# Performance work log

Hardware: AMD Instinct MI355X
Metric: run time of the kernel (lower is better)

The kernel has to match this reference:

```python
import jax, jax.numpy as jnp
import numpy as np

DIM, DEPTH, HEADS = 1024, 6, 16
B, N = 2, 1024
QB = 128.0   # 8-bit activation absmax quant: Qb = 2**(8-1)
EPS = 1e-5


def setup_inputs() -> dict:
    key = jax.random.key(0)
    ks = jax.random.split(key, 4)
    x = jax.random.normal(ks[0], (B, N, DIM), dtype=jnp.float32)
    # BitLinear weights (per layer, two per FFN block), latent fp weights
    ff_w1 = jax.random.normal(ks[1], (DEPTH, DIM, DIM), dtype=jnp.float32) * 0.02
    ff_w2 = jax.random.normal(ks[2], (DEPTH, DIM, DIM), dtype=jnp.float32) * 0.02
    # LayerNorm params (inside FeedForward) and final norm
    ff_ln_g = jnp.ones((DEPTH, DIM), jnp.float32)
    ff_ln_b = jnp.zeros((DEPTH, DIM), jnp.float32)
    final_ln_g = jnp.ones((DIM,), jnp.float32)
    final_ln_b = jnp.zeros((DIM,), jnp.float32)
    return dict(x=x, ff_ln_g=ff_ln_g, ff_ln_b=ff_ln_b, ff_w1=ff_w1,
                ff_w2=ff_w2, final_ln_g=final_ln_g, final_ln_b=final_ln_b)


def layernorm(x, g, b):
    m = jnp.mean(x, axis=-1, keepdims=True)
    v = jnp.mean((x - m) ** 2, axis=-1, keepdims=True)
    return (x - m) * jax.lax.rsqrt(v + EPS) * g + b


def bitlinear(x, w):
    # BitNet b1: binarize weights around their mean, absmax-quantize activations to 8 bits,
    # int-style matmul, then rescale by beta*gamma/Qb.
    alpha = jnp.mean(w)
    w_b = jnp.sign(w - alpha)                 # ternary/binary weights {-1,0,+1}
    beta = jnp.mean(jnp.abs(w))               # ||W||_1 / (n*m)
    gamma = jnp.max(jnp.abs(x))               # activation absmax
    x_q = jnp.clip(x * (QB / gamma), -QB + EPS, QB - EPS)
    y = jnp.einsum('...i,oi->...o', x_q, w_b)
    return y * (beta * gamma / QB)


def attend(x):
    # non-flash multi-head self-attention, q=k=v=x (Attend has no projections)
    b, n, d = x.shape
    dh = d // HEADS
    q = x.reshape(b, n, HEADS, dh).transpose(0, 2, 1, 3)          # bhnd
    scores = jnp.einsum('bhid,bhjd->bhij', q, q) * (dh ** -0.5)   # [B,H,N,N]
    attn = jax.nn.softmax(scores, axis=-1)
    out = jnp.einsum('bhij,bhjd->bhid', attn, q)
    return out.transpose(0, 2, 1, 3).reshape(b, n, d)


def reference(x, ff_ln_g, ff_ln_b, ff_w1, ff_w2, final_ln_g, final_ln_b):
    for i in range(DEPTH):
        x = attend(x) + x
        h = layernorm(x, ff_ln_g[i], ff_ln_b[i])
        h = bitlinear(h, ff_w1[i])
        h = jax.nn.gelu(h, approximate=False)   # torch nn.GELU default = exact
        h = bitlinear(h, ff_w2[i])
        x = h + x
    return layernorm(x, final_ln_g, final_ln_b)
```

## Files before the change

### kernel.cpp

```cpp
#include <hip/hip_runtime.h>
#include <math.h>

typedef __attribute__((ext_vector_type(4))) float f32x4;
typedef __attribute__((ext_vector_type(8))) _Float16 f16x8;

__device__ __forceinline__ f32x4 mfma16h(f16x8 a, f16x8 b, f32x4 c){
  return __builtin_amdgcn_mfma_f32_16x16x32_f16(a, b, c, 0, 0, 0);
}
__device__ __forceinline__ void gload_lds16(const void* g, void* l){
  __builtin_amdgcn_global_load_lds((const __attribute__((address_space(1))) void*)g,
                                   (__attribute__((address_space(3))) void*)l, 16, 0, 0);
}

__global__ __launch_bounds__(256) void k_wstats(const float* __restrict__ w1, const float* __restrict__ w2,
                                                double* __restrict__ dsum, double* __restrict__ dabs){
  const int mat = blockIdx.y;
  const float* wp = (mat < 6) ? (w1 + (size_t)mat*1048576) : (w2 + (size_t)(mat-6)*1048576);
  const f32x4* wv = (const f32x4*)wp + (size_t)blockIdx.x*8192;
  double s = 0.0, a = 0.0;
  for (int j = 0; j < 32; j++){
    f32x4 v = wv[j*256 + threadIdx.x];
    s += (double)v.x + (double)v.y + (double)v.z + (double)v.w;
    a += (double)fabsf(v.x) + (double)fabsf(v.y) + (double)fabsf(v.z) + (double)fabsf(v.w);
  }
  for (int d = 1; d < 64; d <<= 1){ s += __shfl_xor(s, d); a += __shfl_xor(a, d); }
  __shared__ double red[8];
  const int w = threadIdx.x >> 6;
  if ((threadIdx.x & 63) == 0){ red[w*2] = s; red[w*2+1] = a; }
  __syncthreads();
  if (threadIdx.x == 0){
    double S = red[0]+red[2]+red[4]+red[6], A = red[1]+red[3]+red[5]+red[7];
    atomicAdd(&dsum[mat], S);
    atomicAdd(&dabs[mat], A);
  }
}

__global__ __launch_bounds__(256) void k_binarize(const float* __restrict__ w1, const float* __restrict__ w2,
                                                  const double* __restrict__ dsum, _Float16* __restrict__ wb){
  const int blk = blockIdx.x;
  const int mat = blk >> 9;
  const float alpha = (float)(dsum[mat] * (1.0/1048576.0));
  const float* wp = (mat < 6) ? (w1 + (size_t)mat*1048576) : (w2 + (size_t)(mat-6)*1048576);
  const size_t off = (size_t)(blk & 511)*2048 + (size_t)threadIdx.x*8;
  const int n = (int)(off >> 10), k = (int)(off & 1023);
  f32x4 v0 = *(const f32x4*)(wp + off), v1 = *(const f32x4*)(wp + off + 4);
  float vv[8] = {v0.x,v0.y,v0.z,v0.w,v1.x,v1.y,v1.z,v1.w};
  f16x8 pk;
  #pragma unroll
  for (int e = 0; e < 8; e++){
    float d = vv[e] - alpha;
    pk[e] = d > 0.f ? (_Float16)1.0f : (d < 0.f ? (_Float16)(-1.0f) : (_Float16)0.0f);
  }
  const size_t addr = (size_t)mat*1048576 + (size_t)n*1024 + (size_t)((k & ~63) + ((k & 63) ^ ((n&7)*8)));
  *(f16x8*)&wb[addr] = pk;
}

__global__ __launch_bounds__(256) void k_presplit(const float* __restrict__ x,
                                                  _Float16* __restrict__ Kh, _Float16* __restrict__ Kl,
                                                  _Float16* __restrict__ Vh, _Float16* __restrict__ Vl){
  __shared__ _Float16 lh[64*72], ll[64*72];
  const int t = blockIdx.x, bh = blockIdx.y, b = bh>>4, h = bh&15;
  const int n = threadIdx.x>>2, c0 = (threadIdx.x&3)*16;
  const float* src = x + (size_t)b*1048576 + (size_t)(t*64+n)*1024 + h*64 + c0;
  const size_t kbase = ((size_t)bh*1024 + t*64 + n)*64;
  const int sw = (n&7)*8;
  #pragma unroll
  for (int j = 0; j < 2; j++){
    f32x4 v0 = *(const f32x4*)(src + j*8);
    f32x4 v1 = *(const f32x4*)(src + j*8 + 4);
    float vv[8] = {v0.x,v0.y,v0.z,v0.w,v1.x,v1.y,v1.z,v1.w};
    f16x8 Hv, Lv;
    #pragma unroll
    for (int e = 0; e < 8; e++){
      _Float16 hh = (_Float16)vv[e];
      Hv[e] = hh; Lv[e] = (_Float16)(vv[e] - (float)hh);
      const int d = c0 + j*8 + e;
      lh[d*72 + n] = Hv[e]; ll[d*72 + n] = Lv[e];
    }
    const int db = c0 + j*8;
    *(f16x8*)&Kh[kbase + (db ^ sw)] = Hv;
    *(f16x8*)&Kl[kbase + (db ^ sw)] = Lv;
  }
  __syncthreads();
  const int d = threadIdx.x>>2, n0c = (threadIdx.x&3)*16;
  const size_t vbase = ((size_t)bh*64 + d)*1024 + t*64;
  const int sw2 = (d&7)*8;
  #pragma unroll
  for (int j = 0; j < 2; j++){
    f16x8 Hv, Lv;
    #pragma unroll
    for (int e = 0; e < 8; e++){
      Hv[e] = lh[d*72 + n0c + j*8 + e];
      Lv[e] = ll[d*72 + n0c + j*8 + e];
    }
    const int nb = n0c + j*8;
    *(f16x8*)&Vh[vbase + (nb ^ sw2)] = Hv;
    *(f16x8*)&Vl[vbase + (nb ^ sw2)] = Lv;
  }
}

__global__ __launch_bounds__(256) void k_attn(const _Float16* __restrict__ Kh, const _Float16* __restrict__ Kl,
                                              const _Float16* __restrict__ Vh, const _Float16* __restrict__ Vl,
                                              const float* __restrict__ xin, float* __restrict__ xout){
  __shared__ _Float16 smb[24576];
  _Float16* kt_h = smb;
  _Float16* kt_l = smb + 4096;
  _Float16* vt_h = smb + 8192;
  _Float16* vt_l = smb + 12288;
  _Float16* ps_h = smb + 16384;
  _Float16* ps_l = smb + 20480;
  const int tid = threadIdx.x, w = tid>>6, l = tid&63, g = l>>4, r16 = l&15;
  const int bh = blockIdx.x, qt = blockIdx.y, b = bh>>4, h = bh&15;
  const int swr = (r16&7)*8;
  const _Float16* Qsh = Kh + ((size_t)bh*1024 + qt*64)*64;
  const _Float16* Qsl = Kl + ((size_t)bh*1024 + qt*64)*64;
  #pragma unroll
  for (int j = 0; j < 2; j++){
    const int cb = (j*4 + w)*64;
    gload_lds16(Qsh + (size_t)(cb + l)*8, ps_h + cb*8);
    gload_lds16(Qsl + (size_t)(cb + l)*8, ps_l + cb*8);
  }
  __syncthreads();
  const int qrow = w*16 + r16;
  const f16x8 aqh0 = *(const f16x8*)&ps_h[qrow*64 + ((g*8) ^ swr)];
  const f16x8 aqh1 = *(const f16x8*)&ps_h[qrow*64 + ((32 + g*8) ^ swr)];
  const f16x8 aql0 = *(const f16x8*)&ps_l[qrow*64 + ((g*8) ^ swr)];
  const f16x8 aql1 = *(const f16x8*)&ps_l[qrow*64 + ((32 + g*8) ^ swr)];
  __syncthreads();
  float mI[4], lI[4]; f32x4 acc[4];
  #pragma unroll
  for (int i = 0; i < 4; i++){ mI[i] = -1e30f; lI[i] = 0.f; acc[i] = (f32x4){0.f,0.f,0.f,0.f}; }
  const _Float16* Kbh = Kh + (size_t)bh*65536;
  const _Float16* Kbl = Kl + (size_t)bh*65536;
  for (int t = 0; t < 16; t++){
    __syncthreads();
    #pragma unroll
    for (int j = 0; j < 2; j++){
      const int cb = (j*4 + w)*64;
      const int c  = cb + l;
      gload_lds16(Kbh + (size_t)t*4096 + (size_t)c*8, kt_h + cb*8);
      gload_lds16(Kbl + (size_t)t*4096 + (size_t)c*8, kt_l + cb*8);
      gload_lds16(Vh + ((size_t)bh*64 + (c>>3))*1024 + t*64 + (c&7)*8, vt_h + cb*8);
      gload_lds16(Vl + ((size_t)bh*64 + (c>>3))*1024 + t*64 + (c&7)*8, vt_l + cb*8);
    }
    __syncthreads();
    f32x4 s[4];
    #pragma unroll
    for (int c = 0; c < 4; c++){
      const int rk = c*16 + r16;
      const f16x8 kh0 = *(const f16x8*)&kt_h[rk*64 + ((g*8) ^ swr)];
      const f16x8 kh1 = *(const f16x8*)&kt_h[rk*64 + ((32+g*8) ^ swr)];
      const f16x8 kl0 = *(const f16x8*)&kt_l[rk*64 + ((g*8) ^ swr)];
      const f16x8 kl1 = *(const f16x8*)&kt_l[rk*64 + ((32+g*8) ^ swr)];
      f32x4 z = (f32x4){0.f,0.f,0.f,0.f};
      z = mfma16h(aqh0, kh0, z);
      z = mfma16h(aqh1, kh1, z);
      z = mfma16h(aql0, kh0, z);
      z = mfma16h(aql1, kh1, z);
      z = mfma16h(aqh0, kl0, z);
      z = mfma16h(aqh1, kl1, z);
      s[c] = z * 0.125f;
    }
    float rmax[4], rsum[4], fac[4];
    #pragma unroll
    for (int i = 0; i < 4; i++) rmax[i] = fmaxf(fmaxf(s[0][i],s[1][i]), fmaxf(s[2][i],s[3][i]));
    for (int d = 1; d < 16; d <<= 1)
      #pragma unroll
      for (int i = 0; i < 4; i++) rmax[i] = fmaxf(rmax[i], __shfl_xor(rmax[i], d));
    #pragma unroll
    for (int i = 0; i < 4; i++){
      float mn = fmaxf(mI[i], rmax[i]);
      fac[i] = __expf(mI[i] - mn);
      mI[i] = mn; rsum[i] = 0.f;
    }
    #pragma unroll
    for (int c = 0; c < 4; c++)
      #pragma unroll
      for (int i = 0; i < 4; i++){
        float p = __expf(s[c][i] - mI[i]);
        _Float16 ph = (_Float16)p;
        const int prow = w*16 + g*4 + i;
        const int pcol = (c*16 + r16) ^ ((2*g + (i>>1))*8);
        ps_h[prow*64 + pcol] = ph;
        ps_l[prow*64 + pcol] = (_Float16)(p - (float)ph);
        rsum[i] += p;
      }
    for (int d = 1; d < 16; d <<= 1)
      #pragma unroll
      for (int i = 0; i < 4; i++) rsum[i] += __shfl_xor(rsum[i], d);
    #pragma unroll
    for (int i = 0; i < 4; i++) lI[i] = lI[i]*fac[i] + rsum[i];
    #pragma unroll
    for (int dc = 0; dc < 4; dc++)
      #pragma unroll
      for (int i = 0; i < 4; i++) acc[dc][i] *= fac[i];
    const int psw = (r16>>1)*8;
    #pragma unroll
    for (int ks = 0; ks < 2; ks++){
      const f16x8 aph = *(const f16x8*)&ps_h[(w*16+r16)*64 + ((ks*32 + g*8) ^ psw)];
      const f16x8 apl = *(const f16x8*)&ps_l[(w*16+r16)*64 + ((ks*32 + g*8) ^ psw)];
      #pragma unroll
      for (int dc = 0; dc < 4; dc++){
        const int vr = dc*16 + r16;
        const f16x8 bvh = *(const f16x8*)&vt_h[vr*64 + ((ks*32 + g*8) ^ swr)];
        const f16x8 bvl = *(const f16x8*)&vt_l[vr*64 + ((ks*32 + g*8) ^ swr)];
        acc[dc] = mfma16h(aph, bvh, acc[dc]);
        acc[dc] = mfma16h(apl, bvh, acc[dc]);
        acc[dc] = mfma16h(aph, bvl, acc[dc]);
      }
    }
  }
  #pragma unroll
  for (int dc = 0; dc < 4; dc++)
    #pragma unroll
    for (int i = 0; i < 4; i++){
      const int row = qt*64 + w*16 + g*4 + i;
      const size_t idx = (size_t)b*1048576 + (size_t)row*1024 + h*64 + dc*16 + r16;
      xout[idx] = acc[dc][i]/lI[i] + xin[idx];
    }
}

template<int SPLIT>
__global__ __launch_bounds__(256) void k_ln(const float* __restrict__ x, const float* __restrict__ gg,
                                            const float* __restrict__ bb, float* __restrict__ outf,
                                            _Float16* __restrict__ Oh, _Float16* __restrict__ Ol){
  const int row = blockIdx.x*4 + (threadIdx.x>>6);
  const int lane = threadIdx.x & 63;
  const float* xr = x + (size_t)row*1024;
  f32x4 v[4];
  float s = 0.f, q = 0.f;
  #pragma unroll
  for (int c = 0; c < 2; c++){
    v[c*2]   = *(const f32x4*)(xr + c*512 + lane*8);
    v[c*2+1] = *(const f32x4*)(xr + c*512 + lane*8 + 4);
    #pragma unroll
    for (int e = 0; e < 4; e++){
      s += v[c*2][e] + v[c*2+1][e];
      q += v[c*2][e]*v[c*2][e] + v[c*2+1][e]*v[c*2+1][e];
    }
  }
  for (int d = 1; d < 64; d <<= 1){ s += __shfl_xor(s,d); q += __shfl_xor(q,d); }
  const float mean = s * (1.f/1024.f);
  const float var  = q * (1.f/1024.f) - mean*mean;
  const float rstd = rsqrtf(var + 1e-5f);
  #pragma unroll
  for (int c = 0; c < 2; c++){
    const int col = c*512 + lane*8;
    f32x4 g0 = *(const f32x4*)(gg + col), g1 = *(const f32x4*)(gg + col + 4);
    f32x4 b0 = *(const f32x4*)(bb + col), b1 = *(const f32x4*)(bb + col + 4);
    float h[8];
    #pragma unroll
    for (int e = 0; e < 4; e++){
      h[e]   = (v[c*2][e]  -mean)*rstd*g0[e] + b0[e];
      h[e+4] = (v[c*2+1][e]-mean)*rstd*g1[e] + b1[e];
    }
    if (SPLIT){
      f16x8 Hv, Lv;
      #pragma unroll
      for (int e = 0; e < 8; e++){
        _Float16 hh = (_Float16)h[e];
        Hv[e] = hh; Lv[e] = (_Float16)(h[e] - (float)hh);
      }
      const size_t addr = (size_t)row*1024 + c*512 + (lane>>3)*64 + (((lane&7)*8) ^ ((row&7)*8));
      *(f16x8*)&Oh[addr] = Hv;
      *(f16x8*)&Ol[addr] = Lv;
    } else {
      f32x4 o0, o1;
      #pragma unroll
      for (int e = 0; e < 4; e++){ o0[e] = h[e]; o1[e] = h[e+4]; }
      *(f32x4*)(outf + (size_t)row*1024 + col) = o0;
      *(f32x4*)(outf + (size_t)row*1024 + col + 4) = o1;
    }
  }
}

template<int MODE>
__global__ __launch_bounds__(256) void k_gemm(const _Float16* __restrict__ Ah, const _Float16* __restrict__ Al,
                                              const _Float16* __restrict__ Wg,
                                              float* __restrict__ out32,
                                              _Float16* __restrict__ Oh, _Float16* __restrict__ Ol,
                                              const double* __restrict__ dabs_slot){
  __shared__ _Float16 smb[24576];
  const int tid = threadIdx.x, w = tid>>6, l = tid&63, g = l>>4, r16 = l&15;
  const int wm = w>>1, wn = w&1;
  const int n0 = blockIdx.x*64, m0 = blockIdx.y*64;
  const float scale = (float)(*dabs_slot * (1.0/1048576.0));
  const int swr = (r16&7)*8;
  f32x4 acc[2][2] = {};
  #define STAGE(buf, k0) { _Float16* Bp = smb + (buf)*12288;                              \
    _Pragma("unroll")                                                                     \
    for (int j = 0; j < 2; j++){                                                          \
      const int cb = (j*4 + w)*64; const int c = cb + l;                                  \
      const int r = c>>3; const int cc = (c&7)*8;                                         \
      gload_lds16(Ah + (size_t)(m0 + r)*1024 + (k0) + cc, Bp + cb*8);                     \
      gload_lds16(Al + (size_t)(m0 + r)*1024 + (k0) + cc, Bp + 4096 + cb*8);              \
      gload_lds16(Wg + (size_t)(n0 + r)*1024 + (k0) + cc, Bp + 8192 + cb*8);              \
    } }
  STAGE(0, 0);
  __syncthreads();
  for (int t = 0; t < 16; t++){
    if (t < 15) STAGE((t+1)&1, (t+1)*64);
    const _Float16* Bp = smb + (t&1)*12288;
    #pragma unroll
    for (int kk = 0; kk < 2; kk++){
      f16x8 ah[2], al[2], bf[2];
      const int col = (kk*32 + g*8) ^ swr;
      #pragma unroll
      for (int mi = 0; mi < 2; mi++){
        const int row = wm*32 + mi*16 + r16;
        ah[mi] = *(const f16x8*)&Bp[row*64 + col];
        al[mi] = *(const f16x8*)&Bp[4096 + row*64 + col];
      }
      #pragma unroll
      for (int ni = 0; ni < 2; ni++){
        const int row = wn*32 + ni*16 + r16;
        bf[ni] = *(const f16x8*)&Bp[8192 + row*64 + col];
      }
      #pragma unroll
      for (int mi = 0; mi < 2; mi++)
        #pragma unroll
        for (int ni = 0; ni < 2; ni++){
          acc[mi][ni] = mfma16h(ah[mi], bf[ni], acc[mi][ni]);
          acc[mi][ni] = mfma16h(al[mi], bf[ni], acc[mi][ni]);
        }
    }
    __syncthreads();
  }
  #undef STAGE
  #pragma unroll
  for (int mi = 0; mi < 2; mi++)
    #pragma unroll
    for (int ni = 0; ni < 2; ni++)
      #pragma unroll
      for (int i = 0; i < 4; i++){
        const int rr = m0 + wm*32 + mi*16 + g*4 + i;
        const int cc = n0 + wn*32 + ni*16 + r16;
        float vv = acc[mi][ni][i] * scale;
        if (MODE == 0){
          vv = 0.5f*vv*(1.f + erff(vv*0.70710678118f));
          _Float16 hh = (_Float16)vv;
          const size_t addr = (size_t)rr*1024 + (cc & ~63) + ((cc & 63) ^ ((rr&7)*8));
          Oh[addr] = hh;
          Ol[addr] = (_Float16)(vv - (float)hh);
        } else {
          out32[(size_t)rr*1024 + cc] += vv;
        }
      }
}

extern "C" void kernel_launch(void* const* d_in, const int* in_sizes, int n_in,
                              void* d_out, int out_size, void* d_ws, size_t ws_size,
                              hipStream_t stream){
  const float* x_in = (const float*)d_in[0];
  const float* ln_g = (const float*)d_in[1];
  const float* ln_b = (const float*)d_in[2];
  const float* w1   = (const float*)d_in[3];
  const float* w2   = (const float*)d_in[4];
  const float* fg   = (const float*)d_in[5];
  const float* fb   = (const float*)d_in[6];

  char* ws = (char*)d_ws;
  double*   dsum  = (double*)ws;
  double*   dabs  = (double*)(ws + 96);
  _Float16* wb = (_Float16*)(ws + 256);
  size_t o = 256 + 12ull*1048576ull*2ull;
  float* xA = (float*)(ws + o); o += 2048ull*1024*4;
  float* xB = (float*)(ws + o); o += 2048ull*1024*4;
  _Float16* Kh = (_Float16*)(ws + o); o += 2048ull*1024*2;
  _Float16* Kl = (_Float16*)(ws + o); o += 2048ull*1024*2;
  _Float16* Vh = (_Float16*)(ws + o); o += 2048ull*1024*2;
  _Float16* Vl = (_Float16*)(ws + o); o += 2048ull*1024*2;
  _Float16* Ahb = (_Float16*)(ws + o); o += 2048ull*1024*2;
  _Float16* Alb = (_Float16*)(ws + o); o += 2048ull*1024*2;
  _Float16* Ghb = (_Float16*)(ws + o); o += 2048ull*1024*2;
  _Float16* Glb = (_Float16*)(ws + o); o += 2048ull*1024*2;

  hipMemsetAsync(ws, 0, 256, stream);
  k_wstats  <<<dim3(32,12), 256, 0, stream>>>(w1, w2, dsum, dabs);
  k_binarize<<<6144,        256, 0, stream>>>(w1, w2, dsum, wb);

  const float* xc = x_in;
  for (int i = 0; i < 6; i++){
    float* xn = (i & 1) ? xB : xA;
    k_presplit<<<dim3(16,32), 256, 0, stream>>>(xc, Kh, Kl, Vh, Vl);
    k_attn    <<<dim3(32,16), 256, 0, stream>>>(Kh, Kl, Vh, Vl, xc, xn);
    k_ln<1>   <<<512, 256, 0, stream>>>(xn, ln_g + (size_t)i*1024, ln_b + (size_t)i*1024,
                                        nullptr, Ahb, Alb);
    k_gemm<0> <<<dim3(16,32), 256, 0, stream>>>(Ahb, Alb, wb + (size_t)i*1048576,
                                                nullptr, Ghb, Glb, &dabs[i]);
    k_gemm<1> <<<dim3(16,32), 256, 0, stream>>>(Ghb, Glb, wb + (size_t)(6+i)*1048576,
                                                xn, nullptr, nullptr, &dabs[6+i]);
    xc = xn;
  }
  k_ln<0><<<512, 256, 0, stream>>>(xc, fg, fb, (float*)d_out, nullptr, nullptr);
}
```

Before: 581.9 us.

## Split attention over two key segments and merge partials in a combine kernel

Attention now splits the key sequence into two halves across a third grid dimension, doubling the block count from 512 to 1024 so more of the GPU's compute units stay busy. Each block writes an unnormalized partial output and its per-row max and sum, and a new combine kernel merges the two halves with a log-sum-exp rescale and adds the residual. The softmax also switches to exp2 with the scale folded into a single constant. The cost is an extra kernel launch per layer plus a round trip of the partial outputs through global memory.

```diff
diff --git a/kernel.cpp b/kernel.cpp
--- a/kernel.cpp
+++ b/kernel.cpp
@@ -11,6 +11,8 @@
   __builtin_amdgcn_global_load_lds((const __attribute__((address_space(1))) void*)g,
                                    (__attribute__((address_space(3))) void*)l, 16, 0, 0);
 }
+
+#define EXPC 0.1803368801111204f
 
 __global__ __launch_bounds__(256) void k_wstats(const float* __restrict__ w1, const float* __restrict__ w2,
                                                 double* __restrict__ dsum, double* __restrict__ dabs){
@@ -101,7 +103,7 @@
 
 __global__ __launch_bounds__(256) void k_attn(const _Float16* __restrict__ Kh, const _Float16* __restrict__ Kl,
                                               const _Float16* __restrict__ Vh, const _Float16* __restrict__ Vl,
-                                              const float* __restrict__ xin, float* __restrict__ xout){
+                                              float* __restrict__ Op, float* __restrict__ mlb){
   __shared__ _Float16 smb[24576];
   _Float16* kt_h = smb;
   _Float16* kt_l = smb + 4096;
@@ -110,7 +112,7 @@
   _Float16* ps_h = smb + 16384;
   _Float16* ps_l = smb + 20480;
   const int tid = threadIdx.x, w = tid>>6, l = tid&63, g = l>>4, r16 = l&15;
-  const int bh = blockIdx.x, qt = blockIdx.y, b = bh>>4, h = bh&15;
+  const int bh = blockIdx.x, qt = blockIdx.y, kseg = blockIdx.z;
   const int swr = (r16&7)*8;
   const _Float16* Qsh = Kh + ((size_t)bh*1024 + qt*64)*64;
   const _Float16* Qsl = Kl + ((size_t)bh*1024 + qt*64)*64;
@@ -132,7 +134,8 @@
   for (int i = 0; i < 4; i++){ mI[i] = -1e30f; lI[i] = 0.f; acc[i] = (f32x4){0.f,0.f,0.f,0.f}; }
   const _Float16* Kbh = Kh + (size_t)bh*65536;
   const _Float16* Kbl = Kl + (size_t)bh*65536;
-  for (int t = 0; t < 16; t++){
+  for (int tt = 0; tt < 8; tt++){
+    const int t = (kseg<<3) + tt;
     __syncthreads();
     #pragma unroll
     for (int j = 0; j < 2; j++){
@@ -159,9 +162,9 @@
       z = mfma16h(aql1, kh1, z);
       z = mfma16h(aqh0, kl0, z);
       z = mfma16h(aqh1, kl1, z);
-      s[c] = z * 0.125f;
-    }
-    float rmax[4], rsum[4], fac[4];
+      s[c] = z;
+    }
+    float rmax[4], rsum[4], fac[4], mnC[4];
     #pragma unroll
     for (int i = 0; i < 4; i++) rmax[i] = fmaxf(fmaxf(s[0][i],s[1][i]), fmaxf(s[2][i],s[3][i]));
     for (int d = 1; d < 16; d <<= 1)
@@ -170,14 +173,14 @@
     #pragma unroll
     for (int i = 0; i < 4; i++){
       float mn = fmaxf(mI[i], rmax[i]);
-      fac[i] = __expf(mI[i] - mn);
-      mI[i] = mn; rsum[i] = 0.f;
+      fac[i] = exp2f((mI[i] - mn)*EXPC);
+      mI[i] = mn; mnC[i] = mn*EXPC; rsum[i] = 0.f;
     }
     #pragma unroll
     for (int c = 0; c < 4; c++)
       #pragma unroll
       for (int i = 0; i < 4; i++){
-        float p = __expf(s[c][i] - mI[i]);
+        float p = exp2f(fmaf(s[c][i], EXPC, -mnC[i]));
         _Float16 ph = (_Float16)p;
         const int prow = w*16 + g*4 + i;
         const int pcol = (c*16 + r16) ^ ((2*g + (i>>1))*8);
@@ -210,14 +213,46 @@
       }
     }
   }
+  float* Ob = Op + ((size_t)(kseg*32 + bh)*1024 + qt*64)*64;
   #pragma unroll
   for (int dc = 0; dc < 4; dc++)
     #pragma unroll
+    for (int i = 0; i < 4; i++)
+      Ob[(w*16 + g*4 + i)*64 + dc*16 + r16] = acc[dc][i];
+  if (r16 == 0){
+    #pragma unroll
     for (int i = 0; i < 4; i++){
-      const int row = qt*64 + w*16 + g*4 + i;
-      const size_t idx = (size_t)b*1048576 + (size_t)row*1024 + h*64 + dc*16 + r16;
-      xout[idx] = acc[dc][i]/lI[i] + xin[idx];
-    }
+      const size_t rix = (size_t)(kseg*32 + bh)*1024 + qt*64 + w*16 + g*4 + i;
+      mlb[rix*2]   = mI[i]*EXPC;
+      mlb[rix*2+1] = lI[i];
+    }
+  }
+}
+
+__global__ __launch_bounds__(256) void k_combine(const float* __restrict__ Op, const float* __restrict__ mlb,
+                                                 const float* __restrict__ xin, float* __restrict__ xout){
+  const int qt = blockIdx.x, bh = blockIdx.y, b = bh>>4, h = bh&15;
+  const int r = threadIdx.x>>2, c0 = (threadIdx.x&3)*16;
+  const int row = qt*64 + r;
+  const size_t r0 = (size_t)bh*1024 + row;
+  const size_t r1 = (size_t)(32+bh)*1024 + row;
+  const float m0 = mlb[r0*2], l0 = mlb[r0*2+1];
+  const float m1 = mlb[r1*2], l1 = mlb[r1*2+1];
+  const float ms = fmaxf(m0, m1);
+  const float f0 = exp2f(m0 - ms), f1 = exp2f(m1 - ms);
+  const float inv = 1.f/(f0*l0 + f1*l1);
+  const size_t p0 = r0*64 + c0, p1 = r1*64 + c0;
+  const size_t xbase = (size_t)b*1048576 + (size_t)row*1024 + h*64 + c0;
+  #pragma unroll
+  for (int j = 0; j < 4; j++){
+    f32x4 o0 = *(const f32x4*)&Op[p0 + j*4];
+    f32x4 o1 = *(const f32x4*)&Op[p1 + j*4];
+    f32x4 xi = *(const f32x4*)&xin[xbase + j*4];
+    f32x4 ov;
+    #pragma unroll
+    for (int e = 0; e < 4; e++) ov[e] = (f0*o0[e] + f1*o1[e])*inv + xi[e];
+    *(f32x4*)&xout[xbase + j*4] = ov;
+  }
 }
 
 template<int SPLIT>
@@ -374,6 +409,8 @@
   _Float16* Alb = (_Float16*)(ws + o); o += 2048ull*1024*2;
   _Float16* Ghb = (_Float16*)(ws + o); o += 2048ull*1024*2;
   _Float16* Glb = (_Float16*)(ws + o); o += 2048ull*1024*2;
+  float* Op  = (float*)(ws + o); o += 2ull*32*1024*64*4;
+  float* mlb = (float*)(ws + o); o += 2ull*32*1024*2*4;
 
   hipMemsetAsync(ws, 0, 256, stream);
   k_wstats  <<<dim3(32,12), 256, 0, stream>>>(w1, w2, dsum, dabs);
@@ -383,7 +420,8 @@
   for (int i = 0; i < 6; i++){
     float* xn = (i & 1) ? xB : xA;
     k_presplit<<<dim3(16,32), 256, 0, stream>>>(xc, Kh, Kl, Vh, Vl);
-    k_attn    <<<dim3(32,16), 256, 0, stream>>>(Kh, Kl, Vh, Vl, xc, xn);
+    k_attn    <<<dim3(32,16,2), 256, 0, stream>>>(Kh, Kl, Vh, Vl, Op, mlb);
+    k_combine <<<dim3(16,32), 256, 0, stream>>>(Op, mlb, xc, xn);
     k_ln<1>   <<<512, 256, 0, stream>>>(xn, ln_g + (size_t)i*1024, ln_b + (size_t)i*1024,
                                         nullptr, Ahb, Alb);
     k_gemm<0> <<<dim3(16,32), 256, 0, stream>>>(Ahb, Alb, wb + (size_t)i*1048576,
```

Measured after the change: 645.4 us. +10.9%, slower.

## Double-buffer K/V tiles in attention and use lazy exp2 softmax rescaling

Applied to the files above, without the earlier changes.

The attention kernel now keeps two K/V stages in LDS and issues the next tile's global-to-LDS loads at the start of each iteration, so the copy overlaps with the current tile's MFMA work. This replaces the old load-then-barrier pattern, which had two barriers per tile. Softmax now uses exp2 with the 1/8 scale folded into one constant. It rescales the accumulator and running sum only when the row max grows past a threshold, skipping the per-tile rescale multiplies. In exchange, LDS use rises to about 80KB per block, which may lower occupancy, and unnormalized probabilities can reach larger fp16 values before a rescale.

```diff
diff --git a/kernel.cpp b/kernel.cpp
--- a/kernel.cpp
+++ b/kernel.cpp
@@ -11,6 +11,8 @@
   __builtin_amdgcn_global_load_lds((const __attribute__((address_space(1))) void*)g,
                                    (__attribute__((address_space(3))) void*)l, 16, 0, 0);
 }
+
+#define EXPC 0.1803368801111204f
 
 __global__ __launch_bounds__(256) void k_wstats(const float* __restrict__ w1, const float* __restrict__ w2,
                                                 double* __restrict__ dsum, double* __restrict__ dabs){
@@ -102,24 +104,34 @@
 __global__ __launch_bounds__(256) void k_attn(const _Float16* __restrict__ Kh, const _Float16* __restrict__ Kl,
                                               const _Float16* __restrict__ Vh, const _Float16* __restrict__ Vl,
                                               const float* __restrict__ xin, float* __restrict__ xout){
-  __shared__ _Float16 smb[24576];
-  _Float16* kt_h = smb;
-  _Float16* kt_l = smb + 4096;
-  _Float16* vt_h = smb + 8192;
-  _Float16* vt_l = smb + 12288;
-  _Float16* ps_h = smb + 16384;
-  _Float16* ps_l = smb + 20480;
+  __shared__ _Float16 smb[40960];
+  _Float16* ps_h = smb + 32768;
+  _Float16* ps_l = smb + 36864;
   const int tid = threadIdx.x, w = tid>>6, l = tid&63, g = l>>4, r16 = l&15;
   const int bh = blockIdx.x, qt = blockIdx.y, b = bh>>4, h = bh&15;
   const int swr = (r16&7)*8;
-  const _Float16* Qsh = Kh + ((size_t)bh*1024 + qt*64)*64;
-  const _Float16* Qsl = Kl + ((size_t)bh*1024 + qt*64)*64;
+  const _Float16* Kbh = Kh + (size_t)bh*65536;
+  const _Float16* Kbl = Kl + (size_t)bh*65536;
+
+  #define ASTAGE(buf, t) { _Float16* Bp = smb + (buf)*16384;                                    \
+    _Pragma("unroll")                                                                            \
+    for (int j = 0; j < 2; j++){                                                                 \
+      const int cb = (j*4 + w)*64; const int c = cb + l;                                         \
+      gload_lds16(Kbh + (size_t)(t)*4096 + (size_t)c*8, Bp + cb*8);                              \
+      gload_lds16(Kbl + (size_t)(t)*4096 + (size_t)c*8, Bp + 4096 + cb*8);                       \
+      gload_lds16(Vh + ((size_t)bh*64 + (c>>3))*1024 + (t)*64 + (c&7)*8, Bp + 8192 + cb*8);      \
+      gload_lds16(Vl + ((size_t)bh*64 + (c>>3))*1024 + (t)*64 + (c&7)*8, Bp + 12288 + cb*8);     \
+    } }
+
+  const _Float16* Qsh = Kbh + (size_t)qt*4096;
+  const _Float16* Qsl = Kbl + (size_t)qt*4096;
   #pragma unroll
   for (int j = 0; j < 2; j++){
     const int cb = (j*4 + w)*64;
     gload_lds16(Qsh + (size_t)(cb + l)*8, ps_h + cb*8);
     gload_lds16(Qsl + (size_t)(cb + l)*8, ps_l + cb*8);
   }
+  ASTAGE(0, 0);
   __syncthreads();
   const int qrow = w*16 + r16;
   const f16x8 aqh0 = *(const f16x8*)&ps_h[qrow*64 + ((g*8) ^ swr)];
@@ -130,20 +142,13 @@
   float mI[4], lI[4]; f32x4 acc[4];
   #pragma unroll
   for (int i = 0; i < 4; i++){ mI[i] = -1e30f; lI[i] = 0.f; acc[i] = (f32x4){0.f,0.f,0.f,0.f}; }
-  const _Float16* Kbh = Kh + (size_t)bh*65536;
-  const _Float16* Kbl = Kl + (size_t)bh*65536;
+
   for (int t = 0; t < 16; t++){
-    __syncthreads();
-    #pragma unroll
-    for (int j = 0; j < 2; j++){
-      const int cb = (j*4 + w)*64;
-      const int c  = cb + l;
-      gload_lds16(Kbh + (size_t)t*4096 + (size_t)c*8, kt_h + cb*8);
-      gload_lds16(Kbl + (size_t)t*4096 + (size_t)c*8, kt_l + cb*8);
-      gload_lds16(Vh + ((size_t)bh*64 + (c>>3))*1024 + t*64 + (c&7)*8, vt_h + cb*8);
-      gload_lds16(Vl + ((size_t)bh*64 + (c>>3))*1024 + t*64 + (c&7)*8, vt_l + cb*8);
-    }
-    __syncthreads();
+    if (t < 15) ASTAGE((t+1)&1, t+1);
+    const _Float16* kt_h = smb + (t&1)*16384;
+    const _Float16* kt_l = kt_h + 4096;
+    const _Float16* vt_h = kt_h + 8192;
+    const _Float16* vt_l = kt_h + 12288;
     f32x4 s[4];
     #pragma unroll
     for (int c = 0; c < 4; c++){
@@ -159,25 +164,33 @@
       z = mfma16h(aql1, kh1, z);
       z = mfma16h(aqh0, kl0, z);
       z = mfma16h(aqh1, kl1, z);
-      s[c] = z * 0.125f;
-    }
-    float rmax[4], rsum[4], fac[4];
+      s[c] = z;
+    }
+    float rmax[4], rsum[4], mnC[4];
     #pragma unroll
     for (int i = 0; i < 4; i++) rmax[i] = fmaxf(fmaxf(s[0][i],s[1][i]), fmaxf(s[2][i],s[3][i]));
     for (int d = 1; d < 16; d <<= 1)
       #pragma unroll
       for (int i = 0; i < 4; i++) rmax[i] = fmaxf(rmax[i], __shfl_xor(rmax[i], d));
-    #pragma unroll
-    for (int i = 0; i < 4; i++){
-      float mn = fmaxf(mI[i], rmax[i]);
-      fac[i] = __expf(mI[i] - mn);
-      mI[i] = mn; rsum[i] = 0.f;
-    }
+    const float dmax = fmaxf(fmaxf(rmax[0]-mI[0], rmax[1]-mI[1]), fmaxf(rmax[2]-mI[2], rmax[3]-mI[3]));
+    if (dmax > 44.36f){
+      #pragma unroll
+      for (int i = 0; i < 4; i++){
+        const float mn = fmaxf(mI[i], rmax[i]);
+        const float fac = exp2f((mI[i] - mn)*EXPC);
+        lI[i] *= fac;
+        mI[i] = mn;
+        #pragma unroll
+        for (int dc = 0; dc < 4; dc++) acc[dc][i] *= fac;
+      }
+    }
+    #pragma unroll
+    for (int i = 0; i < 4; i++){ mnC[i] = mI[i]*EXPC; rsum[i] = 0.f; }
     #pragma unroll
     for (int c = 0; c < 4; c++)
       #pragma unroll
       for (int i = 0; i < 4; i++){
-        float p = __expf(s[c][i] - mI[i]);
+        float p = exp2f(fmaf(s[c][i], EXPC, -mnC[i]));
         _Float16 ph = (_Float16)p;
         const int prow = w*16 + g*4 + i;
         const int pcol = (c*16 + r16) ^ ((2*g + (i>>1))*8);
@@ -189,11 +202,7 @@
       #pragma unroll
       for (int i = 0; i < 4; i++) rsum[i] += __shfl_xor(rsum[i], d);
     #pragma unroll
-    for (int i = 0; i < 4; i++) lI[i] = lI[i]*fac[i] + rsum[i];
-    #pragma unroll
-    for (int dc = 0; dc < 4; dc++)
-      #pragma unroll
-      for (int i = 0; i < 4; i++) acc[dc][i] *= fac[i];
+    for (int i = 0; i < 4; i++) lI[i] += rsum[i];
     const int psw = (r16>>1)*8;
     #pragma unroll
     for (int ks = 0; ks < 2; ks++){
@@ -209,7 +218,9 @@
         acc[dc] = mfma16h(aph, bvl, acc[dc]);
       }
     }
-  }
+    __syncthreads();
+  }
+  #undef ASTAGE
   #pragma unroll
   for (int dc = 0; dc < 4; dc++)
     #pragma unroll
```

Result: slower. 596.3 us (+2.5%).
